# Kernel optimization log

Measured on AMD Instinct MI355X. Metric: run time of the kernel, lower is better.

The kernel has to match this reference:

```python
import jax, jax.numpy as jnp
import numpy as np

D_MODEL = 2048
N_HEADS = 8
N_KV = 4
HEAD_DIM = 256
WINDOW = 1024
EPS = 1e-6
ROPE_BASE = 10000.0


def _rms_norm(x, w):
    # x: [..., D]; matches torch: x * rsqrt(mean(x^2) + eps) * w
    return x * jax.lax.rsqrt(jnp.mean(x * x, axis=-1, keepdims=True) + EPS) * w


def _rope_cos_sin(pos):
    # pos: [T] ints -> cos/sin: [T, HEAD_DIM] (cat(freqs, freqs) as in source)
    inv_freq = 1.0 / (ROPE_BASE ** (jnp.arange(0, HEAD_DIM, 2, dtype=jnp.float32) / HEAD_DIM))
    freqs = pos.astype(jnp.float32)[:, None] * inv_freq[None, :]  # [T, D/2]
    emb = jnp.concatenate([freqs, freqs], axis=-1)                # [T, D]
    return jnp.cos(emb), jnp.sin(emb)


def _apply_rotary(x, cos, sin):
    # x: [B, H, T, D]; interleaved rotate-half exactly as the torch code
    x1 = x[..., 0::2]
    x2 = x[..., 1::2]
    x_rot = jnp.stack([-x2, x1], axis=-1).reshape(x.shape)
    return x * cos[None, None, :, :] + x_rot * sin[None, None, :, :]


def setup_inputs() -> dict:
    key = jax.random.key(0)
    ks = jax.random.split(key, 8)
    B, T = 1, 4096
    s = 0.02
    return {
        "x": jax.random.normal(ks[0], (B, T, D_MODEL), dtype=jnp.float32),
        "pos": jnp.arange(T, dtype=jnp.int32),
        "Wq": jax.random.normal(ks[1], (N_HEADS * HEAD_DIM, D_MODEL), dtype=jnp.float32) * s,
        "Wk": jax.random.normal(ks[2], (N_KV * HEAD_DIM, D_MODEL), dtype=jnp.float32) * s,
        "Wv": jax.random.normal(ks[3], (N_KV * HEAD_DIM, D_MODEL), dtype=jnp.float32) * s,
        "Wo": jax.random.normal(ks[4], (D_MODEL, N_HEADS * HEAD_DIM), dtype=jnp.float32) * s,
        "q_norm_w": jnp.ones((HEAD_DIM,), dtype=jnp.float32),
        "k_norm_w": jnp.ones((HEAD_DIM,), dtype=jnp.float32),
    }


def reference(x, pos, Wq, Wk, Wv, Wo, q_norm_w, k_norm_w):
    B, T, _ = x.shape
    # projections (torch Linear: y = x @ W.T)
    q = (x @ Wq.T).reshape(B, T, N_HEADS, HEAD_DIM).transpose(0, 2, 1, 3)  # [B,H,T,D]
    k = (x @ Wk.T).reshape(B, T, N_KV, HEAD_DIM).transpose(0, 2, 1, 3)    # [B,Hkv,T,D]
    v = (x @ Wv.T).reshape(B, T, N_KV, HEAD_DIM).transpose(0, 2, 1, 3)
    # per-head RMSNorm
    q = _rms_norm(q, q_norm_w)
    k = _rms_norm(k, k_norm_w)
    # RoPE
    cos, sin = _rope_cos_sin(pos)
    q = _apply_rotary(q, cos, sin)
    k = _apply_rotary(k, cos, sin)
    # GQA repeat: [B,Hkv,T,D] -> [B,H,T,D]
    rep = N_HEADS // N_KV
    k = jnp.repeat(k, rep, axis=1)
    v = jnp.repeat(v, rep, axis=1)
    # full scores + sliding-window causal mask (faithful to source)
    scores = jnp.einsum("bhqd,bhkd->bhqk", q, k) / jnp.sqrt(jnp.float32(HEAD_DIM))
    i = jnp.arange(T)[:, None]
    j = jnp.arange(T)[None, :]
    allowed = (j <= i) & (j >= i - WINDOW + 1)  # [T,T]
    scores = jnp.where(allowed[None, None, :, :], scores, -jnp.inf)
    attn = jax.nn.softmax(scores, axis=-1)
    y = jnp.einsum("bhqk,bhkd->bhqd", attn, v)
    y = y.transpose(0, 2, 1, 3).reshape(B, T, N_HEADS * HEAD_DIM)
    return y @ Wo.T
```

## Files before the change

### kernel.cpp

```cpp
#include <hip/hip_runtime.h>
#include <cstdint>
#include <cmath>

typedef __bf16 bf16x8 __attribute__((ext_vector_type(8)));
typedef float  f32x4  __attribute__((ext_vector_type(4)));

#define DEVI __device__ __forceinline__

#define SEQ 4096
#define NH 8
#define NKV 4
#define HD 256
#define WIN 1024

DEVI void gload16(const void* g, void* l) {
  __builtin_amdgcn_global_load_lds((const __attribute__((address_space(1))) void*)g,
                                   (__attribute__((address_space(3))) void*)l,
                                   16, 0, 0);
}

DEVI bf16x8 ld8f(const float* p) {
  const f32x4 a = *(const f32x4*)p;
  const f32x4 b = *(const f32x4*)(p + 4);
  bf16x8 r;
#pragma unroll
  for (int j = 0; j < 4; ++j) { r[j] = (__bf16)a[j]; r[4 + j] = (__bf16)b[j]; }
  return r;
}

DEVI void st1(float* p, float v)  { *p = v; }
DEVI void st1(__bf16* p, float v) { *p = (__bf16)v; }

DEVI void barx() {
  asm volatile("" ::: "memory");
  __builtin_amdgcn_s_barrier();
  asm volatile("" ::: "memory");
}

__global__ __launch_bounds__(256)
void cvt_all(const float* __restrict__ x,  const float* __restrict__ wq,
             const float* __restrict__ wk, const float* __restrict__ wv,
             const float* __restrict__ wo,
             __bf16* __restrict__ xb, __bf16* __restrict__ wqkvb,
             __bf16* __restrict__ wob) {
  const size_t g = (size_t)blockIdx.x * 256 + threadIdx.x;
  const float* src; __bf16* dst; size_t off;
  if      (g < 1048576) { src = x;  dst = xb;               off = g; }
  else if (g < 1572864) { src = wq; dst = wqkvb;            off = g - 1048576; }
  else if (g < 1835008) { src = wk; dst = wqkvb + 4194304;  off = g - 1572864; }
  else if (g < 2097152) { src = wv; dst = wqkvb + 6291456;  off = g - 1835008; }
  else                  { src = wo; dst = wob;              off = g - 2097152; }
  *(bf16x8*)(dst + off * 8) = ld8f(src + off * 8);
}

template <int BM, typename TC>
__global__ __launch_bounds__(512, 2)
void gemm256(const __bf16* __restrict__ A, const __bf16* __restrict__ B,
             TC* __restrict__ C, int N, int K) {
  constexpr int AI    = BM / 128;
  constexpr int MF    = BM / 32;
  constexpr int AUNIT = BM * 64;
  constexpr int ASZ   = 4 * AUNIT;
  constexpr int VMC   = 2 * (AI + 2);
  __shared__ char lds[ASZ + 65536];

  const int tid  = threadIdx.x;
  const int lane = tid & 63;
  const int wave = tid >> 6;
  const int l15  = lane & 15;
  const int l4   = lane >> 4;
  const int wm   = wave >> 2;
  const int wn   = wave & 3;

  constexpr int nTm = 4096 / BM;
  const int lin  = blockIdx.x;
  const int xcd  = lin & 7;
  const int kk   = lin >> 3;
  const int nTn  = N >> 8;
  const int rowT = kk % nTm;
  const int colT = xcd * (nTn >> 3) + kk / nTm;
  const int row0 = rowT * BM;
  const int col0 = colT << 8;

  const int srow = tid >> 2;
  const int scol = ((tid & 3) ^ ((tid >> 3) & 3)) << 3;
  const __bf16* Asrc = A + (size_t)(row0 + srow) * K + scol;
  const __bf16* Bsrc = B + (size_t)(col0 + srow) * K + scol;

  const int swz  = (l4 ^ ((l15 >> 1) & 3)) << 4;
  const int aoff = (wm * (BM / 2) + l15) * 64 + swz;
  const int boff = ((wn << 6) + l15) * 64 + swz;

  auto stA = [&](int kx, int h, int b) {
    int k0 = kx << 6; if (k0 >= K) k0 = 0;
    const __bf16* s = Asrc + k0 + (h << 5);
    char* d = lds + (b * 2 + h) * AUNIT + wave * 1024;
#pragma unroll
    for (int i = 0; i < AI; ++i)
      gload16(s + (size_t)(i << 7) * K, d + i * 8192);
  };
  auto stB = [&](int kx, int h, int b) {
    int k0 = kx << 6; if (k0 >= K) k0 = 0;
    const __bf16* s = Bsrc + k0 + (h << 5);
    char* d = lds + ASZ + (b * 2 + h) * 16384 + wave * 1024;
#pragma unroll
    for (int i = 0; i < 2; ++i)
      gload16(s + (size_t)(i << 7) * K, d + i * 8192);
  };

  f32x4 acc[MF][4] = {};

  stA(0, 0, 0); stB(0, 0, 0);
  stA(0, 1, 0); stB(0, 1, 0);
  stA(1, 0, 1); stB(1, 0, 1);

  const int NT = K >> 6;
  for (int kt = 0; kt < NT; ++kt) {
    const int b = kt & 1, nb = b ^ 1;
#pragma unroll
    for (int half = 0; half < 2; ++half) {
      asm volatile("s_waitcnt vmcnt(%0)" :: "i"(VMC) : "memory");
      barx();
      bf16x8 af[4], ag[4], bfr[4];
      const char* pa = lds + (b * 2 + half) * AUNIT + aoff;
      const char* pb = lds + ASZ + (b * 2 + half) * 16384 + boff;
#pragma unroll
      for (int m = 0; m < 4; ++m) af[m] = *(const bf16x8*)(pa + (m << 10));
#pragma unroll
      for (int n = 0; n < 4; ++n) bfr[n] = *(const bf16x8*)(pb + (n << 10));
      if constexpr (BM == 256) {
#pragma unroll
        for (int m = 0; m < 4; ++m) ag[m] = *(const bf16x8*)(pa + 4096 + (m << 10));
      }
      if (half == 0) { stA(kt + 1, 1, nb); stB(kt + 1, 1, nb); }
      else           { stA(kt + 2, 0, b);  stB(kt + 2, 0, b);  }
      __builtin_amdgcn_s_setprio(1);
#pragma unroll
      for (int m = 0; m < 4; ++m)
#pragma unroll
        for (int n = 0; n < 4; ++n)
          acc[m][n] = __builtin_amdgcn_mfma_f32_16x16x32_bf16(af[m], bfr[n], acc[m][n], 0, 0, 0);
      if constexpr (BM == 256) {
#pragma unroll
        for (int m = 0; m < 4; ++m)
#pragma unroll
          for (int n = 0; n < 4; ++n)
            acc[4 + m][n] = __builtin_amdgcn_mfma_f32_16x16x32_bf16(ag[m], bfr[n], acc[4 + m][n], 0, 0, 0);
      }
      __builtin_amdgcn_s_setprio(0);
    }
  }

#pragma unroll
  for (int mf = 0; mf < MF; ++mf) {
    const int rb = row0 + wm * (BM / 2) + (mf >> 2) * 64 + (mf & 3) * 16 + (l4 << 2);
#pragma unroll
    for (int reg = 0; reg < 4; ++reg) {
      TC* crow = C + (size_t)(rb + reg) * N + col0 + (wn << 6) + l15;
#pragma unroll
      for (int n = 0; n < 4; ++n) st1(crow + (n << 4), acc[mf][n][reg]);
    }
  }
}

__global__ __launch_bounds__(256)
void norm_rope_tv(__bf16* __restrict__ qkv, __bf16* __restrict__ Vt,
                  const float* __restrict__ qw, const float* __restrict__ kw,
                  const int* __restrict__ pos) {
  if (blockIdx.x < 12288) {
    const int gw   = blockIdx.x * 4 + (threadIdx.x >> 6);
    const int lane = threadIdx.x & 63;
    __bf16* base; const float* w; int t;
    if (gw < SEQ * NH) {
      t = gw >> 3;
      base = qkv + (size_t)t * 4096 + (gw & 7) * HD;
      w = qw;
    } else {
      const int g = gw - SEQ * NH;
      t = g >> 2;
      base = qkv + (size_t)t * 4096 + 2048 + (g & 3) * HD;
      w = kw;
    }

    const int d0 = lane * 4;
    float v[4]; float ss = 0.f;
#pragma unroll
    for (int j = 0; j < 4; ++j) { v[j] = (float)base[d0 + j]; ss += v[j] * v[j]; }
#pragma unroll
    for (int off = 1; off < 64; off <<= 1) ss += __shfl_xor(ss, off);
    const float rms = rsqrtf(ss * (1.0f / 256.0f) + 1e-6f);
    const float p = (float)pos[t];

    float n[4];
#pragma unroll
    for (int j = 0; j < 4; ++j) n[j] = v[j] * rms * w[d0 + j];

    float outv[4];
#pragma unroll
    for (int e = 0; e < 4; e += 2) {
      const int i0 = d0 + e, i1 = i0 + 1;
      const float f0 = exp2f(-(float)(i0 & 127) * 0.103810253f);
      const float f1 = exp2f(-(float)(i1 & 127) * 0.103810253f);
      float s0, cc0, s1, cc1;
      sincosf(p * f0, &s0, &cc0);
      sincosf(p * f1, &s1, &cc1);
      outv[e]     = n[e] * cc0 - n[e + 1] * s0;
      outv[e + 1] = n[e + 1] * cc1 + n[e] * s1;
    }
#pragma unroll
    for (int j = 0; j < 4; ++j) base[d0 + j] = (__bf16)outv[j];
  } else {
    __shared__ __bf16 tile[64][72];
    const int b   = blockIdx.x - 12288;
    const int tid = threadIdx.x;
    const int tb  = (b & 63) * 64;
    const int yy  = b >> 6;
    const int kvh = yy >> 2;
    const int db  = (yy & 3) * 64;
#pragma unroll
    for (int i = 0; i < 2; ++i) {
      const int s = i * 256 + tid;
      const int r = s >> 3, c = (s & 7) * 8;
      bf16x8 val = *(const bf16x8*)(qkv + (size_t)(tb + r) * 4096 + 3072 + kvh * HD + db + c);
#pragma unroll
      for (int j = 0; j < 8; ++j) tile[r][c + j] = val[j];
    }
    __syncthreads();
#pragma unroll
    for (int i = 0; i < 2; ++i) {
      const int s = i * 256 + tid;
      const int r = s >> 3, c = (s & 7) * 8;
      bf16x8 outv;
#pragma unroll
      for (int j = 0; j < 8; ++j) outv[j] = tile[c + j][r];
      *(bf16x8*)(Vt + (size_t)(kvh * HD + db + r) * SEQ + tb + c) = outv;
    }
  }
}

__global__ __launch_bounds__(256, 2)
void attn_fwd(const __bf16* __restrict__ qkv, const __bf16* __restrict__ Vt,
              __bf16* __restrict__ Y) {
  __shared__ char klds[2][16384];
  __shared__ char vlds[2][16384];
  __shared__ __bf16 Ps[4][16][40];
  const int tid  = threadIdx.x;
  const int lane = tid & 63;
  const int wave = tid >> 6;
  const int l15  = lane & 15;
  const int l4   = lane >> 4;
  const int lin  = blockIdx.x;
  const int head = lin & 7;
  const int q0   = (lin >> 3) * 64;
  const int kvh  = head >> 1;
  const int qw   = q0 + wave * 16;

  bf16x8 qf[8];
  const __bf16* qrow = qkv + (size_t)(qw + l15) * 4096 + head * HD;
#pragma unroll
  for (int ks = 0; ks < 8; ++ks) {
    bf16x8 t = *(const bf16x8*)(qrow + ks * 32 + l4 * 8);
#pragma unroll
    for (int j = 0; j < 8; ++j) t[j] = (__bf16)((float)t[j] * 0.0625f);
    qf[ks] = t;
  }

  f32x4 o[16] = {};
  float l_run[4] = {0.f, 0.f, 0.f, 0.f};

  int lo = q0 - (WIN - 1); if (lo < 0) lo = 0;
  const int kt0 = lo >> 5;
  const int kt1 = (q0 + 63) >> 5;
  const int kbmax = kt1 << 5;

  const int skey = (tid >> 2) & 31;
  const int sdim = tid >> 2;
  const int sg   = (tid & 3) ^ ((tid >> 3) & 3);
  const int sth  = tid >> 7;

  auto stK = [&](int kt, int b) {
    int kb = kt << 5; if (kb > kbmax) kb = kbmax;
    const __bf16* s = qkv + (size_t)(kb + skey) * 4096 + 2048 + kvh * HD
                          + sth * 32 + sg * 8;
    char* d = klds[b] + wave * 1024;
#pragma unroll
    for (int i = 0; i < 4; ++i)
      gload16(s + i * 64, d + i * 4096);
  };
  auto stV = [&](int kt, int b) {
    int kb = kt << 5; if (kb > kbmax) kb = kbmax;
    const __bf16* s = Vt + ((size_t)kvh * HD + sdim) * SEQ + kb + sg * 8;
    char* d = vlds[b] + wave * 1024;
#pragma unroll
    for (int i = 0; i < 4; ++i)
      gload16(s + (size_t)i * 64 * SEQ, d + i * 4096);
  };

  stK(kt0, 0);     stV(kt0, 0);
  stK(kt0 + 1, 1); stV(kt0 + 1, 1);

  const int rswz = (l4 ^ ((l15 >> 1) & 3)) << 4;

  for (int kt = kt0; kt <= kt1; ++kt) {
    const int p  = (kt - kt0) & 1;
    const int kb = kt << 5;
    asm volatile("s_waitcnt vmcnt(8)" ::: "memory");
    barx();

    const char* kbase = klds[p];
    f32x4 s_acc[2] = {};
    __builtin_amdgcn_s_setprio(1);
#pragma unroll
    for (int kn = 0; kn < 2; ++kn) {
#pragma unroll
      for (int ks = 0; ks < 8; ++ks) {
        bf16x8 kf = *(const bf16x8*)(kbase + (ks * 32 + kn * 16 + l15) * 64 + rswz);
        s_acc[kn] = __builtin_amdgcn_mfma_f32_16x16x32_bf16(qf[ks], kf, s_acc[kn], 0, 0, 0);
      }
    }
    __builtin_amdgcn_s_setprio(0);

#pragma unroll
    for (int reg = 0; reg < 4; ++reg) {
      const int r  = l4 * 4 + reg;
      const int qg = qw + r;
      float ps = 0.f;
#pragma unroll
      for (int kn = 0; kn < 2; ++kn) {
        const int kg = kb + kn * 16 + l15;
        const bool ok = (kg <= qg) && (kg > qg - WIN);
        const float pv = ok ? __expf(fminf(s_acc[kn][reg], 34.f) - 34.f) : 0.f;
        ps += pv;
        Ps[wave][r][kn * 16 + l15] = (__bf16)pv;
      }
      l_run[reg] += ps;
    }

    const char* vbase = vlds[p];
    bf16x8 pf = *(const bf16x8*)&Ps[wave][l15][l4 * 8];
    __builtin_amdgcn_s_setprio(1);
#pragma unroll
    for (int dn = 0; dn < 16; ++dn) {
      bf16x8 vf = *(const bf16x8*)(vbase + (dn * 16 + l15) * 64 + rswz);
      o[dn] = __builtin_amdgcn_mfma_f32_16x16x32_bf16(pf, vf, o[dn], 0, 0, 0);
    }
    __builtin_amdgcn_s_setprio(0);

    barx();
    stK(kt + 2, p);
    stV(kt + 2, p);
  }
  asm volatile("s_waitcnt vmcnt(0)" ::: "memory");

#pragma unroll
  for (int reg = 0; reg < 4; ++reg) {
#pragma unroll
    for (int off = 1; off < 16; off <<= 1)
      l_run[reg] += __shfl_xor(l_run[reg], off);
    const float inv = 1.0f / l_run[reg];
    const int q = qw + l4 * 4 + reg;
    __bf16* yrow = Y + ((size_t)q * NH + head) * HD + l15;
#pragma unroll
    for (int dn = 0; dn < 16; ++dn)
      yrow[dn * 16] = (__bf16)(o[dn][reg] * inv);
  }
}

extern "C" void kernel_launch(void* const* d_in, const int* in_sizes, int n_in,
                              void* d_out, int out_size, void* d_ws, size_t ws_size,
                              hipStream_t stream) {
  (void)in_sizes; (void)n_in; (void)out_size; (void)ws_size;
  const float* x   = (const float*)d_in[0];
  const int*   pos = (const int*)d_in[1];
  const float* Wq  = (const float*)d_in[2];
  const float* Wk  = (const float*)d_in[3];
  const float* Wv  = (const float*)d_in[4];
  const float* Wo  = (const float*)d_in[5];
  const float* qw  = (const float*)d_in[6];
  const float* kw  = (const float*)d_in[7];
  float* out = (float*)d_out;

  char* ws = (char*)d_ws;
  const size_t MB = 1024 * 1024;
  __bf16* qkv_ws = (__bf16*)(ws);
  __bf16* vt_ws  = (__bf16*)(ws + 32 * MB);
  __bf16* y_ws   = (__bf16*)(ws + 40 * MB);
  __bf16* xb     = (__bf16*)(ws + 56 * MB);
  __bf16* wqkvb  = (__bf16*)(ws + 72 * MB);
  __bf16* wob    = (__bf16*)(ws + 88 * MB);

  cvt_all<<<dim3(10240), dim3(256), 0, stream>>>(x, Wq, Wk, Wv, Wo, xb, wqkvb, wob);
  gemm256<256, __bf16><<<dim3(256), dim3(512), 0, stream>>>(xb, wqkvb, qkv_ws, 4096, 2048);
  norm_rope_tv<<<dim3(13312), dim3(256), 0, stream>>>(qkv_ws, vt_ws, qw, kw, pos);
  attn_fwd<<<dim3(512), dim3(256), 0, stream>>>(qkv_ws, vt_ws, y_ws);
  gemm256<128, float><<<dim3(256), dim3(512), 0, stream>>>(y_ws, wob, out, 2048, 2048);
}
```

Measured before the change: 317.2 us.

## Split GEMM k-step into four ping-pong phases interleaving LDS reads, prefetch, MFMA

Restructures the bf16 GEMM main loop so each k-tile half is processed as two M-groups, with LDS fragment reads, global-to-LDS prefetch issue, and MFMA bursts interleaved and a barrier before each MFMA group. Buffer selection is derived from the k index, and the vmcnt waits are placed mid-step. The aim is to overlap memory traffic with matrix math more finely and cut register pressure from holding all A fragments at once. It adds more barriers per iteration and tighter synchronization, and the correctness of the LDS overwrite timing depends on the barrier placement.

After: 324.9 us. 1.02x slower.

```diff
diff --git a/kernel.cpp b/kernel.cpp
--- a/kernel.cpp
+++ b/kernel.cpp
@@ -59,9 +59,10 @@
              TC* __restrict__ C, int N, int K) {
   constexpr int AI    = BM / 128;
   constexpr int MF    = BM / 32;
+  constexpr int MH    = MF / 2;
   constexpr int AUNIT = BM * 64;
   constexpr int ASZ   = 4 * AUNIT;
-  constexpr int VMC   = 2 * (AI + 2);
+  constexpr int VMC   = 2 * AI + 4;
   __shared__ char lds[ASZ + 65536];
 
   const int tid  = threadIdx.x;
@@ -91,18 +92,18 @@
   const int aoff = (wm * (BM / 2) + l15) * 64 + swz;
   const int boff = ((wn << 6) + l15) * 64 + swz;
 
-  auto stA = [&](int kx, int h, int b) {
+  auto stA = [&](int kx, int h) {
     int k0 = kx << 6; if (k0 >= K) k0 = 0;
     const __bf16* s = Asrc + k0 + (h << 5);
-    char* d = lds + (b * 2 + h) * AUNIT + wave * 1024;
+    char* d = lds + ((kx & 1) * 2 + h) * AUNIT + wave * 1024;
 #pragma unroll
     for (int i = 0; i < AI; ++i)
       gload16(s + (size_t)(i << 7) * K, d + i * 8192);
   };
-  auto stB = [&](int kx, int h, int b) {
+  auto stB = [&](int kx, int h) {
     int k0 = kx << 6; if (k0 >= K) k0 = 0;
     const __bf16* s = Bsrc + k0 + (h << 5);
-    char* d = lds + ASZ + (b * 2 + h) * 16384 + wave * 1024;
+    char* d = lds + ASZ + ((kx & 1) * 2 + h) * 16384 + wave * 1024;
 #pragma unroll
     for (int i = 0; i < 2; ++i)
       gload16(s + (size_t)(i << 7) * K, d + i * 8192);
@@ -110,46 +111,56 @@
 
   f32x4 acc[MF][4] = {};
 
-  stA(0, 0, 0); stB(0, 0, 0);
-  stA(0, 1, 0); stB(0, 1, 0);
-  stA(1, 0, 1); stB(1, 0, 1);
+  stA(0, 0); stB(0, 0); stA(0, 1); stB(0, 1); stA(1, 0); stB(1, 0);
+  asm volatile("s_waitcnt vmcnt(%0)" :: "i"(VMC) : "memory");
+  barx();
 
   const int NT = K >> 6;
   for (int kt = 0; kt < NT; ++kt) {
-    const int b = kt & 1, nb = b ^ 1;
-#pragma unroll
-    for (int half = 0; half < 2; ++half) {
-      asm volatile("s_waitcnt vmcnt(%0)" :: "i"(VMC) : "memory");
+    const int bb = (kt & 1) * 2;
+    bf16x8 bfr[4];
+    bf16x8 af[MH];
+
+    auto rd = [&](int h, int mg, bool readB) {
+      const char* pa = lds + (bb + h) * AUNIT + aoff;
+#pragma unroll
+      for (int m = 0; m < MH; ++m)
+        af[m] = *(const bf16x8*)(pa + ((mg * MH + m) << 10));
+      if (readB) {
+        const char* pb = lds + ASZ + (bb + h) * 16384 + boff;
+#pragma unroll
+        for (int n = 0; n < 4; ++n)
+          bfr[n] = *(const bf16x8*)(pb + (n << 10));
+      }
+    };
+    auto mm = [&](int mg) {
       barx();
-      bf16x8 af[4], ag[4], bfr[4];
-      const char* pa = lds + (b * 2 + half) * AUNIT + aoff;
-      const char* pb = lds + ASZ + (b * 2 + half) * 16384 + boff;
-#pragma unroll
-      for (int m = 0; m < 4; ++m) af[m] = *(const bf16x8*)(pa + (m << 10));
-#pragma unroll
-      for (int n = 0; n < 4; ++n) bfr[n] = *(const bf16x8*)(pb + (n << 10));
-      if constexpr (BM == 256) {
-#pragma unroll
-        for (int m = 0; m < 4; ++m) ag[m] = *(const bf16x8*)(pa + 4096 + (m << 10));
-      }
-      if (half == 0) { stA(kt + 1, 1, nb); stB(kt + 1, 1, nb); }
-      else           { stA(kt + 2, 0, b);  stB(kt + 2, 0, b);  }
       __builtin_amdgcn_s_setprio(1);
 #pragma unroll
-      for (int m = 0; m < 4; ++m)
+      for (int m = 0; m < MH; ++m)
 #pragma unroll
         for (int n = 0; n < 4; ++n)
-          acc[m][n] = __builtin_amdgcn_mfma_f32_16x16x32_bf16(af[m], bfr[n], acc[m][n], 0, 0, 0);
-      if constexpr (BM == 256) {
-#pragma unroll
-        for (int m = 0; m < 4; ++m)
-#pragma unroll
-          for (int n = 0; n < 4; ++n)
-            acc[4 + m][n] = __builtin_amdgcn_mfma_f32_16x16x32_bf16(ag[m], bfr[n], acc[4 + m][n], 0, 0, 0);
-      }
+          acc[mg * MH + m][n] =
+              __builtin_amdgcn_mfma_f32_16x16x32_bf16(af[m], bfr[n], acc[mg * MH + m][n], 0, 0, 0);
       __builtin_amdgcn_s_setprio(0);
-    }
-  }
+    };
+
+    rd(0, 0, true);
+    stA(kt + 1, 1);
+    mm(0);
+    rd(0, 1, false);
+    stB(kt + 1, 1);
+    asm volatile("s_waitcnt vmcnt(%0)" :: "i"(VMC) : "memory");
+    mm(1);
+    rd(1, 0, true);
+    stA(kt + 2, 0);
+    mm(0);
+    rd(1, 1, false);
+    stB(kt + 2, 0);
+    asm volatile("s_waitcnt vmcnt(%0)" :: "i"(VMC) : "memory");
+    mm(1);
+  }
+  asm volatile("s_waitcnt vmcnt(0)" ::: "memory");
 
 #pragma unroll
   for (int mf = 0; mf < MF; ++mf) {
```
